# Kernel optimization log

Measured on AMD Instinct MI355X. Metric: run time of the kernel, lower is better.

The kernel has to match this reference:

```python
import jax, jax.numpy as jnp
import numpy as np

B, N, D = 256, 128, 128            # batch, tree nodes (incl. zero-pad node 0), input_feature_dim
MAX_PRED, MAX_COL, MAX_OP = 30, 200, 20
OTHER = D - 2 * MAX_PRED - 1 - 32  # 35
C_IN = D + 64 - 2 * MAX_PRED - 1   # 131 = tree-conv input channels


def setup_inputs() -> dict:
    key = jax.random.key(0)
    ks = jax.random.split(key, 14)
    others = jax.random.normal(ks[0], (B, N, OTHER), dtype=jnp.float32)
    cols = jax.random.randint(ks[1], (B, N, MAX_PRED), 0, MAX_COL).astype(jnp.float32)
    ops = jax.random.randint(ks[2], (B, N, MAX_PRED), 0, MAX_OP).astype(jnp.float32)
    length = jax.random.randint(ks[3], (B, N, 1), 0, MAX_PRED + 1).astype(jnp.float32)
    param = jax.random.normal(ks[4], (B, N, 32), dtype=jnp.float32)
    feature = jnp.concatenate([others, cols, ops, length, param], axis=-1).transpose(0, 2, 1)  # (B, D, N)
    indexes = jax.random.randint(ks[5], (B, 3 * (N - 1), 1), 0, N, dtype=jnp.int32).astype(jnp.int64)

    def conv_w(k, o, i):
        return jax.random.normal(k, (o, i, 3), dtype=jnp.float32) * (1.0 / np.sqrt(3 * i))

    def lin_w(k, o, i):
        return jax.random.normal(k, (o, i), dtype=jnp.float32) * (1.0 / np.sqrt(i))

    return dict(
        feature=feature, indexes=indexes,
        col_embed=jax.random.normal(ks[6], (MAX_COL, 32), dtype=jnp.float32),
        op_embed=jax.random.normal(ks[7], (MAX_OP, 32), dtype=jnp.float32),
        w1=conv_w(ks[8], 256, C_IN), b1=jnp.zeros((256,), jnp.float32),
        w2=conv_w(ks[9], 128, 256), b2=jnp.zeros((128,), jnp.float32),
        w3=conv_w(ks[10], 64, 128), b3=jnp.zeros((64,), jnp.float32),
        fw1=lin_w(ks[11], 32, 64), fb1=jnp.zeros((32,), jnp.float32),
        fw2=lin_w(ks[12], 1, 32), fb2=jnp.zeros((1,), jnp.float32),
    )


def tree_conv(x, idx, w, b):
    # x: (B, C, N); idx: (B, 3M, 1) with M = N-1; w: (O, C, 3)
    Bb, C, _ = x.shape
    g = jnp.take_along_axis(x, idx[:, :, 0][:, None, :], axis=2)        # (B, C, 3M) gather (self,left,right)
    g = g.reshape(Bb, C, -1, 3)                                          # (B, C, M, 3)
    out = jnp.einsum('bcmk,ock->bom', g, w) + b[None, :, None]           # stride-3 kernel-3 conv
    zero = jnp.zeros((Bb, w.shape[0], 1), out.dtype)                     # re-prepend zero-pad node
    return jnp.concatenate([zero, out], axis=2)                          # (B, O, N)


def tree_norm(x):
    # per-sample layernorm over (channel, node) dims, unbiased std (torch.std default)
    mean = jnp.mean(x, axis=(1, 2), keepdims=True)
    std = jnp.std(x, axis=(1, 2), ddof=1, keepdims=True)
    return (x - mean) / (std + 1e-5)


def reference(feature, indexes, col_embed, op_embed, w1, b1, w2, b2, w3, b3, fw1, fb1, fw2, fb2):
    Bb, d, n = feature.shape
    f = feature.transpose(0, 2, 1).reshape(Bb * n, d)
    others = f[:, :OTHER]
    cols = jax.lax.stop_gradient(f[:, OTHER:OTHER + MAX_PRED]).astype(jnp.int32)
    ops = jax.lax.stop_gradient(f[:, OTHER + MAX_PRED:OTHER + 2 * MAX_PRED]).astype(jnp.int32)
    length = f[:, OTHER + 2 * MAX_PRED:OTHER + 2 * MAX_PRED + 1]          # (BN, 1)
    param = f[:, -32:]
    emb = jnp.concatenate([col_embed[cols], op_embed[ops]], axis=-1)      # (BN, P, 64)
    mask = jnp.arange(MAX_PRED)[None, :] < length                         # (BN, P)
    total = jnp.sum(emb * mask[..., None], axis=1)                        # (BN, 64) masked sum
    collate = jnp.concatenate([others, total, param], axis=-1).reshape(Bb, n, -1).transpose(0, 2, 1)  # (B, C_IN, N)

    x = jax.nn.leaky_relu(tree_norm(tree_conv(collate, indexes, w1, b1)), 0.01)
    x = jax.nn.leaky_relu(tree_norm(tree_conv(x, indexes, w2, b2)), 0.01)
    x = tree_norm(tree_conv(x, indexes, w3, b3))                          # (B, 64, N)
    pooled = jnp.max(x, axis=2)                                           # DynamicPooling -> (B, 64)
    h = jax.nn.relu(pooled @ fw1.T + fb1)
    return h @ fw2.T + fb2                                                # (B, 1)
```

## Files before the change

### kernel.cpp

```cpp
#include <hip/hip_runtime.h>
#include <hip/hip_bf16.h>
#include <math.h>

#define B_    256
#define N_    128
#define MAXP  30
#define OTHER_ 35
#define CIN1  131
#define NIDX  381

#define KPAD1 160
#define KPAD2 256
#define KPAD3 128
#define S_IDX (B_ * NIDX)
#define S_P1  (15 * 4 * 4 * 512)
#define S_P2  (24 * 4 * 2 * 512)
#define S_P3  (12 * 4 * 1 * 512)
#define PREP_TOTAL (S_IDX + S_P1 + S_P2 + S_P3)
#define PREP_BLOCKS ((PREP_TOTAL + 511) / 512)

typedef short short8 __attribute__((ext_vector_type(8)));
typedef float f32x4 __attribute__((ext_vector_type(4)));

__device__ inline void split1(float v, short& h, short& l) {
  unsigned u = __float_as_uint(v);
  unsigned hb = (u + 0x7fffu + ((u >> 16) & 1u)) >> 16;
  float fh = __uint_as_float(hb << 16);
  float r = v - fh;
  unsigned u2 = __float_as_uint(r);
  unsigned lb = (u2 + 0x7fffu + ((u2 >> 16) & 1u)) >> 16;
  h = (short)hb;
  l = (short)lb;
}

__device__ inline void split2(float v, short& h, short& l) {
  __hip_bfloat16 hb = __float2bfloat16(v);
  float fh = __bfloat162float(hb);
  __hip_bfloat16 lb = __float2bfloat16(v - fh);
  __builtin_memcpy(&h, &hb, 2);
  __builtin_memcpy(&l, &lb, 2);
}

template <int KREAL, int KPAD, int SUB, int NWO>
__device__ inline void packw(int l, const float* __restrict__ w,
                             short* __restrict__ oh, short* __restrict__ ol) {
  const int e = l & 7;
  const int lane = (l >> 3) & 63;
  const int x = l >> 9;
  const int su = x % SUB;
  const int y = x / SUB;
  const int g = y % NWO;
  const int gks = y / NWO;
  const int oc = (g * SUB + su) * 16 + (lane & 15);
  const int ctot = gks * 32 + ((lane >> 4) & 3) * 8 + e;
  const int kk = ctot / KPAD;
  const int ch = ctot - kk * KPAD;
  const float v = (ch < KREAL) ? w[(oc * KREAL + ch) * 3 + kk] : 0.f;
  short h, lo;
  split1(v, h, lo);
  oh[l] = h;
  ol[l] = lo;
}

__global__ __launch_bounds__(512) void prep_kernel(
    const void* __restrict__ rawIdx, int* __restrict__ idx32,
    const float* __restrict__ w1, short* __restrict__ w1h, short* __restrict__ w1l,
    const float* __restrict__ w2, short* __restrict__ w2h, short* __restrict__ w2l,
    const float* __restrict__ w3, short* __restrict__ w3h, short* __restrict__ w3l) {
  const int gid = blockIdx.x * 512 + threadIdx.x;
  if (gid < S_IDX) {
    const int* r32 = (const int*)rawIdx;
    const int lane = threadIdx.x & 63;
    const int lo = r32[2 * lane];
    const int hi = r32[2 * lane + 1];
    const bool ok = (hi == 0 && lo >= 0 && lo < N_);
    const bool is64 = __all(ok);
    idx32[gid] = is64 ? (int)((const long long*)rawIdx)[gid] : ((const int*)rawIdx)[gid];
  } else if (gid < S_IDX + S_P1) {
    packw<131, KPAD1, 4, 4>(gid - S_IDX, w1, w1h, w1l);
  } else if (gid < S_IDX + S_P1 + S_P2) {
    packw<256, KPAD2, 2, 4>(gid - (S_IDX + S_P1), w2, w2h, w2l);
  } else if (gid < PREP_TOTAL) {
    packw<128, KPAD3, 1, 4>(gid - (S_IDX + S_P1 + S_P2), w3, w3h, w3l);
  }
}

__global__ __launch_bounds__(1024, 1) void fused_kernel(
    const float* __restrict__ feature,
    const float* __restrict__ col_embed,
    const float* __restrict__ op_embed,
    const int* __restrict__ idx,
    const short* __restrict__ w1h, const short* __restrict__ w1l,
    const short* __restrict__ w2h, const short* __restrict__ w2l,
    const short* __restrict__ w3h, const short* __restrict__ w3l,
    const float* __restrict__ b1, const float* __restrict__ b2,
    const float* __restrict__ b3,
    const float* __restrict__ fw1, const float* __restrict__ fb1,
    const float* __restrict__ fw2, const float* __restrict__ fb2,
    float* __restrict__ out) {
  constexpr int CINP = 264;

  __shared__ short smem[128 * CINP * 2];
  __shared__ int nb_s[NIDX];
  __shared__ double red[32];
  __shared__ float bc[2];
  __shared__ float poolw[16][16];

  short* sH = smem;
  short* sL = smem + 128 * CINP;
  float* feat = (float*)smem;
  float* ceL  = ((float*)smem) + 128 * 133;
  float* oeL  = ceL + 200 * 32;

  const int b = blockIdx.x;
  const int tid = threadIdx.x;
  const int lane = tid & 63;
  const int w = tid >> 6;
  const int wj = w >> 2;
  const int wo = w & 3;
  const int col = lane & 15;
  const int grp = (lane >> 4) & 3;
  const int jbase = wj * 32;
  const int cl = lane & 31;

  const short8* __restrict__ wp1h = (const short8*)w1h;
  const short8* __restrict__ wp1l = (const short8*)w1l;
  const short8* __restrict__ wp2h = (const short8*)w2h;
  const short8* __restrict__ wp2l = (const short8*)w2l;
  const short8* __restrict__ wp3h = (const short8*)w3h;
  const short8* __restrict__ wp3l = (const short8*)w3l;

  auto blockStats = [&](double ss, double sq, double cnt) {
#pragma unroll
    for (int o = 32; o > 0; o >>= 1) {
      ss += __shfl_down(ss, o, 64);
      sq += __shfl_down(sq, o, 64);
    }
    if (lane == 0) { red[w * 2] = ss; red[w * 2 + 1] = sq; }
    __syncthreads();
    if (tid == 0) {
      double S = 0.0, Q = 0.0;
#pragma unroll
      for (int i = 0; i < 16; ++i) { S += red[i * 2]; Q += red[i * 2 + 1]; }
      const double m = S / cnt;
      double var = (Q - S * S / cnt) / (cnt - 1.0);
      if (var < 0.0) var = 0.0;
      bc[0] = (float)m;
      bc[1] = (float)(1.0 / (sqrt(var) + 1e-5));
    }
    __syncthreads();
  };

  {
    const float* fb = feature + (size_t)b * 16384;
#pragma unroll
    for (int it = 0; it < 4; ++it) {
      const int t = it * 1024 + tid;
      const int d = t >> 5;
      const int c4 = (t & 31) * 4;
      const float4 v = *reinterpret_cast<const float4*>(&fb[d * 128 + c4]);
      float* p = &feat[d * 133 + c4];
      p[0] = v.x; p[1] = v.y; p[2] = v.z; p[3] = v.w;
    }
    const float4* s = (const float4*)col_embed;
    float4* d4 = (float4*)ceL;
#pragma unroll
    for (int it = 0; it < 2; ++it) {
      const int t = it * 1024 + tid;
      if (t < 1600) d4[t] = s[t];
    }
    if (tid < 160) ((float4*)oeL)[tid] = ((const float4*)op_embed)[tid];
    if (tid < NIDX) nb_s[tid] = idx[b * NIDX + tid];
  }
  __syncthreads();

  float emb[8], oth[8], par[8];
#pragma unroll
  for (int ni = 0; ni < 8; ++ni) {
    const int n = w * 8 + ni;
    int civ = 0, oiv = 0;
    if (lane < MAXP) civ = (int)feat[(OTHER_ + lane) * 133 + n];
    if (lane >= 32 && lane < 32 + MAXP) oiv = (int)feat[(OTHER_ + MAXP + (lane - 32)) * 133 + n];
    const int L = (int)feat[95 * 133 + n];
    float acc = 0.f;
    for (int i = 0; i < L; ++i) {
      const int cv = __shfl(civ, i);
      const int ov = __shfl(oiv, 32 + i);
      acc += (lane < 32) ? ceL[cv * 32 + cl] : oeL[ov * 32 + cl];
    }
    emb[ni] = acc;
    oth[ni] = (lane < 35) ? feat[lane * 133 + n] : 0.f;
    par[ni] = (lane < 32) ? feat[(96 + lane) * 133 + n] : 0.f;
  }
  int nbr[2][3];
#pragma unroll
  for (int jt = 0; jt < 2; ++jt) {
    const int jA = jbase + jt * 16 + col;
#pragma unroll
    for (int kk = 0; kk < 3; ++kk)
      nbr[jt][kk] = (jA > 0) ? nb_s[(jA - 1) * 3 + kk] : 0;
  }
  __syncthreads();

#pragma unroll
  for (int ni = 0; ni < 8; ++ni) {
    const int n = w * 8 + ni;
    const int base = n * CINP;
    short h, l;
    split2(emb[ni], h, l);
    sH[base + 35 + lane] = h; sL[base + 35 + lane] = l;
    if (lane < 35) {
      split2(oth[ni], h, l);
      sH[base + lane] = h; sL[base + lane] = l;
    }
    if (lane < 32) {
      split2(par[ni], h, l);
      sH[base + 99 + lane] = h; sL[base + 99 + lane] = l;
    }
    if (lane < 29) { sH[base + 131 + lane] = 0; sL[base + 131 + lane] = 0; }
  }
  __syncthreads();

  f32x4 a1[2][4];
#pragma unroll
  for (int jt = 0; jt < 2; ++jt)
#pragma unroll
    for (int su = 0; su < 4; ++su) {
      a1[jt][su][0] = 0.f; a1[jt][su][1] = 0.f;
      a1[jt][su][2] = 0.f; a1[jt][su][3] = 0.f;
    }

#pragma unroll
  for (int kk = 0; kk < 3; ++kk) {
#pragma unroll
    for (int ks = 0; ks < 5; ++ks) {
      const int gks = kk * 5 + ks;
      short8 ah[2], al[2];
#pragma unroll
      for (int jt = 0; jt < 2; ++jt) {
        const int ei = nbr[jt][kk] * CINP + ks * 32 + grp * 8;
        ah[jt] = *reinterpret_cast<const short8*>(&sH[ei]);
        al[jt] = *reinterpret_cast<const short8*>(&sL[ei]);
      }
      short8 bh[4], bl[4];
#pragma unroll
      for (int su = 0; su < 4; ++su) {
        const int wi = ((gks * 4 + wo) * 4 + su) * 64 + lane;
        bh[su] = wp1h[wi];
        bl[su] = wp1l[wi];
      }
#pragma unroll
      for (int jt = 0; jt < 2; ++jt)
#pragma unroll
        for (int su = 0; su < 4; ++su) {
          a1[jt][su] = __builtin_amdgcn_mfma_f32_16x16x32_bf16(ah[jt], bh[su], a1[jt][su], 0, 0, 0);
          a1[jt][su] = __builtin_amdgcn_mfma_f32_16x16x32_bf16(al[jt], bh[su], a1[jt][su], 0, 0, 0);
          a1[jt][su] = __builtin_amdgcn_mfma_f32_16x16x32_bf16(ah[jt], bl[su], a1[jt][su], 0, 0, 0);
        }
    }
  }

  {
    double ss = 0.0, sq = 0.0;
#pragma unroll
    for (int su = 0; su < 4; ++su) {
      const float bv = b1[(wo * 4 + su) * 16 + col];
#pragma unroll
      for (int jt = 0; jt < 2; ++jt)
#pragma unroll
        for (int r = 0; r < 4; ++r) {
          const int j = jbase + jt * 16 + grp * 4 + r;
          const float val = (j > 0) ? a1[jt][su][r] + bv : 0.f;
          a1[jt][su][r] = val;
          ss += (double)val;
          sq += (double)val * (double)val;
        }
    }
    blockStats(ss, sq, 256.0 * 128.0);
  }
  const float mean1 = bc[0], inv1 = bc[1];

#pragma unroll
  for (int su = 0; su < 4; ++su) {
    const int c = (wo * 4 + su) * 16 + col;
#pragma unroll
    for (int jt = 0; jt < 2; ++jt)
#pragma unroll
      for (int r = 0; r < 4; ++r) {
        const int j = jbase + jt * 16 + grp * 4 + r;
        float v = (a1[jt][su][r] - mean1) * inv1;
        v = fmaxf(v, 0.01f * v);
        short h, l;
        split2(v, h, l);
        sH[j * CINP + c] = h;
        sL[j * CINP + c] = l;
      }
  }
  __syncthreads();

  f32x4 a2[2][2];
#pragma unroll
  for (int jt = 0; jt < 2; ++jt)
#pragma unroll
    for (int su = 0; su < 2; ++su) {
      a2[jt][su][0] = 0.f; a2[jt][su][1] = 0.f;
      a2[jt][su][2] = 0.f; a2[jt][su][3] = 0.f;
    }

#pragma unroll
  for (int kk = 0; kk < 3; ++kk) {
#pragma unroll
    for (int ks = 0; ks < 8; ++ks) {
      const int gks = kk * 8 + ks;
      short8 ah[2], al[2];
#pragma unroll
      for (int jt = 0; jt < 2; ++jt) {
        const int ei = nbr[jt][kk] * CINP + ks * 32 + grp * 8;
        ah[jt] = *reinterpret_cast<const short8*>(&sH[ei]);
        al[jt] = *reinterpret_cast<const short8*>(&sL[ei]);
      }
      short8 bh[2], bl[2];
#pragma unroll
      for (int su = 0; su < 2; ++su) {
        const int wi = ((gks * 4 + wo) * 2 + su) * 64 + lane;
        bh[su] = wp2h[wi];
        bl[su] = wp2l[wi];
      }
#pragma unroll
      for (int jt = 0; jt < 2; ++jt)
#pragma unroll
        for (int su = 0; su < 2; ++su) {
          a2[jt][su] = __builtin_amdgcn_mfma_f32_16x16x32_bf16(ah[jt], bh[su], a2[jt][su], 0, 0, 0);
          a2[jt][su] = __builtin_amdgcn_mfma_f32_16x16x32_bf16(al[jt], bh[su], a2[jt][su], 0, 0, 0);
          a2[jt][su] = __builtin_amdgcn_mfma_f32_16x16x32_bf16(ah[jt], bl[su], a2[jt][su], 0, 0, 0);
        }
    }
  }

  {
    double ss = 0.0, sq = 0.0;
#pragma unroll
    for (int su = 0; su < 2; ++su) {
      const float bv = b2[(wo * 2 + su) * 16 + col];
#pragma unroll
      for (int jt = 0; jt < 2; ++jt)
#pragma unroll
        for (int r = 0; r < 4; ++r) {
          const int j = jbase + jt * 16 + grp * 4 + r;
          const float val = (j > 0) ? a2[jt][su][r] + bv : 0.f;
          a2[jt][su][r] = val;
          ss += (double)val;
          sq += (double)val * (double)val;
        }
    }
    blockStats(ss, sq, 128.0 * 128.0);
  }
  const float mean2 = bc[0], inv2 = bc[1];

#pragma unroll
  for (int su = 0; su < 2; ++su) {
    const int c = (wo * 2 + su) * 16 + col;
#pragma unroll
    for (int jt = 0; jt < 2; ++jt)
#pragma unroll
      for (int r = 0; r < 4; ++r) {
        const int j = jbase + jt * 16 + grp * 4 + r;
        float v = (a2[jt][su][r] - mean2) * inv2;
        v = fmaxf(v, 0.01f * v);
        short h, l;
        split2(v, h, l);
        sH[j * CINP + c] = h;
        sL[j * CINP + c] = l;
      }
  }
  __syncthreads();

  f32x4 a3[2];
#pragma unroll
  for (int jt = 0; jt < 2; ++jt) {
    a3[jt][0] = 0.f; a3[jt][1] = 0.f; a3[jt][2] = 0.f; a3[jt][3] = 0.f;
  }

#pragma unroll
  for (int kk = 0; kk < 3; ++kk) {
#pragma unroll
    for (int ks = 0; ks < 4; ++ks) {
      const int gks = kk * 4 + ks;
      short8 ah[2], al[2];
#pragma unroll
      for (int jt = 0; jt < 2; ++jt) {
        const int ei = nbr[jt][kk] * CINP + ks * 32 + grp * 8;
        ah[jt] = *reinterpret_cast<const short8*>(&sH[ei]);
        al[jt] = *reinterpret_cast<const short8*>(&sL[ei]);
      }
      short8 bh, bl;
      {
        const int wi = (gks * 4 + wo) * 64 + lane;
        bh = wp3h[wi];
        bl = wp3l[wi];
      }
#pragma unroll
      for (int jt = 0; jt < 2; ++jt) {
        a3[jt] = __builtin_amdgcn_mfma_f32_16x16x32_bf16(ah[jt], bh, a3[jt], 0, 0, 0);
        a3[jt] = __builtin_amdgcn_mfma_f32_16x16x32_bf16(al[jt], bh, a3[jt], 0, 0, 0);
        a3[jt] = __builtin_amdgcn_mfma_f32_16x16x32_bf16(ah[jt], bl, a3[jt], 0, 0, 0);
      }
    }
  }

  {
    double ss = 0.0, sq = 0.0;
    const float bv = b3[wo * 16 + col];
#pragma unroll
    for (int jt = 0; jt < 2; ++jt)
#pragma unroll
      for (int r = 0; r < 4; ++r) {
        const int j = jbase + jt * 16 + grp * 4 + r;
        const float val = (j > 0) ? a3[jt][r] + bv : 0.f;
        a3[jt][r] = val;
        ss += (double)val;
        sq += (double)val * (double)val;
      }
    blockStats(ss, sq, 64.0 * 128.0);
  }
  const float mean3 = bc[0], inv3 = bc[1];

  {
    float pm = -3.4e38f;
#pragma unroll
    for (int jt = 0; jt < 2; ++jt)
#pragma unroll
      for (int r = 0; r < 4; ++r)
        pm = fmaxf(pm, (a3[jt][r] - mean3) * inv3);
    pm = fmaxf(pm, __shfl_xor(pm, 16, 64));
    pm = fmaxf(pm, __shfl_xor(pm, 32, 64));
    if (lane < 16) poolw[w][col] = pm;
  }
  __syncthreads();

  if (w == 0) {
    float hval = 0.f;
    if (lane < 32) {
      float a = fb1[lane];
#pragma unroll 8
      for (int c = 0; c < 64; ++c) {
        const int oq = c >> 4, oc16 = c & 15;
        float p = poolw[oq][oc16];
#pragma unroll
        for (int jw = 1; jw < 4; ++jw) p = fmaxf(p, poolw[jw * 4 + oq][oc16]);
        a = fmaf(p, fw1[lane * 64 + c], a);
      }
      hval = fmaxf(a, 0.f) * fw2[lane];
    }
#pragma unroll
    for (int o = 32; o > 0; o >>= 1) hval += __shfl_down(hval, o, 64);
    if (lane == 0) out[b] = hval + fb2[0];
  }
}

extern "C" void kernel_launch(void* const* d_in, const int* in_sizes, int n_in,
                              void* d_out, int out_size, void* d_ws, size_t ws_size,
                              hipStream_t stream) {
  const float* feature   = (const float*)d_in[0];
  const void*  indexes   = d_in[1];
  const float* col_embed = (const float*)d_in[2];
  const float* op_embed  = (const float*)d_in[3];
  const float* w1  = (const float*)d_in[4];
  const float* b1  = (const float*)d_in[5];
  const float* w2  = (const float*)d_in[6];
  const float* b2  = (const float*)d_in[7];
  const float* w3  = (const float*)d_in[8];
  const float* b3  = (const float*)d_in[9];
  const float* fw1 = (const float*)d_in[10];
  const float* fb1 = (const float*)d_in[11];
  const float* fw2 = (const float*)d_in[12];
  const float* fb2 = (const float*)d_in[13];
  float* out = (float*)d_out;

  char* ws = (char*)d_ws;
  size_t off = 0;
  auto carve = [&](size_t bytes) -> char* {
    off = (off + 255) & ~(size_t)255;
    char* p = ws + off;
    off += bytes;
    return p;
  };
  int*   idx32 = (int*)carve((size_t)S_IDX * sizeof(int));
  short* w1h   = (short*)carve((size_t)S_P1 * sizeof(short));
  short* w1l   = (short*)carve((size_t)S_P1 * sizeof(short));
  short* w2h   = (short*)carve((size_t)S_P2 * sizeof(short));
  short* w2l   = (short*)carve((size_t)S_P2 * sizeof(short));
  short* w3h   = (short*)carve((size_t)S_P3 * sizeof(short));
  short* w3l   = (short*)carve((size_t)S_P3 * sizeof(short));
  (void)ws_size; (void)in_sizes; (void)n_in; (void)out_size;

  hipLaunchKernelGGL(prep_kernel, dim3(PREP_BLOCKS), dim3(512), 0, stream,
                     indexes, idx32, w1, w1h, w1l, w2, w2h, w2l, w3, w3h, w3l);
  hipLaunchKernelGGL(fused_kernel, dim3(B_), dim3(1024), 0, stream,
                     feature, col_embed, op_embed, idx32,
                     w1h, w1l, w2h, w2l, w3h, w3l,
                     b1, b2, b3, fw1, fb1, fw2, fb2, out);
}
```

Before: 79.41 us.

## Retile warps to 8 node-groups by 2 output-channel groups

The warp-to-tile mapping changes from 4 node blocks × 4 output-channel blocks (32 nodes each) to 8 node blocks × 2 output-channel blocks (16 nodes each). The weight packing layout is changed to match. Each warp now loads one gathered A fragment per k-step and reuses it across more output tiles, which cuts shared-memory gather reads. The trade-off is that each warp fetches twice as many weight fragments from global or L2 memory. The pooling reduction and final MLP indexing are rewritten for the new layout.

```diff
diff --git a/kernel.cpp b/kernel.cpp
--- a/kernel.cpp
+++ b/kernel.cpp
@@ -13,9 +13,9 @@
 #define KPAD2 256
 #define KPAD3 128
 #define S_IDX (B_ * NIDX)
-#define S_P1  (15 * 4 * 4 * 512)
-#define S_P2  (24 * 4 * 2 * 512)
-#define S_P3  (12 * 4 * 1 * 512)
+#define S_P1  (15 * 2 * 8 * 512)
+#define S_P2  (24 * 2 * 4 * 512)
+#define S_P3  (12 * 2 * 2 * 512)
 #define PREP_TOTAL (S_IDX + S_P1 + S_P2 + S_P3)
 #define PREP_BLOCKS ((PREP_TOTAL + 511) / 512)
 
@@ -77,11 +77,11 @@
     const bool is64 = __all(ok);
     idx32[gid] = is64 ? (int)((const long long*)rawIdx)[gid] : ((const int*)rawIdx)[gid];
   } else if (gid < S_IDX + S_P1) {
-    packw<131, KPAD1, 4, 4>(gid - S_IDX, w1, w1h, w1l);
+    packw<131, KPAD1, 8, 2>(gid - S_IDX, w1, w1h, w1l);
   } else if (gid < S_IDX + S_P1 + S_P2) {
-    packw<256, KPAD2, 2, 4>(gid - (S_IDX + S_P1), w2, w2h, w2l);
+    packw<256, KPAD2, 4, 2>(gid - (S_IDX + S_P1), w2, w2h, w2l);
   } else if (gid < PREP_TOTAL) {
-    packw<128, KPAD3, 1, 4>(gid - (S_IDX + S_P1 + S_P2), w3, w3h, w3l);
+    packw<128, KPAD3, 2, 2>(gid - (S_IDX + S_P1 + S_P2), w3, w3h, w3l);
   }
 }
 
@@ -104,7 +104,7 @@
   __shared__ int nb_s[NIDX];
   __shared__ double red[32];
   __shared__ float bc[2];
-  __shared__ float poolw[16][16];
+  __shared__ float poolw[16][32];
 
   short* sH = smem;
   short* sL = smem + 128 * CINP;
@@ -116,11 +116,11 @@
   const int tid = threadIdx.x;
   const int lane = tid & 63;
   const int w = tid >> 6;
-  const int wj = w >> 2;
-  const int wo = w & 3;
+  const int wj = w >> 1;
+  const int wo = w & 1;
   const int col = lane & 15;
   const int grp = (lane >> 4) & 3;
-  const int jbase = wj * 32;
+  const int jbase = wj * 16;
   const int cl = lane & 31;
 
   const short8* __restrict__ wp1h = (const short8*)w1h;
@@ -192,13 +192,12 @@
     oth[ni] = (lane < 35) ? feat[lane * 133 + n] : 0.f;
     par[ni] = (lane < 32) ? feat[(96 + lane) * 133 + n] : 0.f;
   }
-  int nbr[2][3];
-#pragma unroll
-  for (int jt = 0; jt < 2; ++jt) {
-    const int jA = jbase + jt * 16 + col;
+  int nbr[3];
+  {
+    const int jA = jbase + col;
 #pragma unroll
     for (int kk = 0; kk < 3; ++kk)
-      nbr[jt][kk] = (jA > 0) ? nb_s[(jA - 1) * 3 + kk] : 0;
+      nbr[kk] = (jA > 0) ? nb_s[(jA - 1) * 3 + kk] : 0;
   }
   __syncthreads();
 
@@ -221,119 +220,166 @@
   }
   __syncthreads();
 
-  f32x4 a1[2][4];
-#pragma unroll
-  for (int jt = 0; jt < 2; ++jt)
-#pragma unroll
-    for (int su = 0; su < 4; ++su) {
-      a1[jt][su][0] = 0.f; a1[jt][su][1] = 0.f;
-      a1[jt][su][2] = 0.f; a1[jt][su][3] = 0.f;
-    }
+  f32x4 a1[8];
+#pragma unroll
+  for (int su = 0; su < 8; ++su) {
+    a1[su][0] = 0.f; a1[su][1] = 0.f; a1[su][2] = 0.f; a1[su][3] = 0.f;
+  }
 
 #pragma unroll
   for (int kk = 0; kk < 3; ++kk) {
 #pragma unroll
     for (int ks = 0; ks < 5; ++ks) {
       const int gks = kk * 5 + ks;
-      short8 ah[2], al[2];
-#pragma unroll
-      for (int jt = 0; jt < 2; ++jt) {
-        const int ei = nbr[jt][kk] * CINP + ks * 32 + grp * 8;
-        ah[jt] = *reinterpret_cast<const short8*>(&sH[ei]);
-        al[jt] = *reinterpret_cast<const short8*>(&sL[ei]);
-      }
-      short8 bh[4], bl[4];
-#pragma unroll
-      for (int su = 0; su < 4; ++su) {
-        const int wi = ((gks * 4 + wo) * 4 + su) * 64 + lane;
-        bh[su] = wp1h[wi];
-        bl[su] = wp1l[wi];
-      }
-#pragma unroll
-      for (int jt = 0; jt < 2; ++jt)
-#pragma unroll
-        for (int su = 0; su < 4; ++su) {
-          a1[jt][su] = __builtin_amdgcn_mfma_f32_16x16x32_bf16(ah[jt], bh[su], a1[jt][su], 0, 0, 0);
-          a1[jt][su] = __builtin_amdgcn_mfma_f32_16x16x32_bf16(al[jt], bh[su], a1[jt][su], 0, 0, 0);
-          a1[jt][su] = __builtin_amdgcn_mfma_f32_16x16x32_bf16(ah[jt], bl[su], a1[jt][su], 0, 0, 0);
+      const int ei = nbr[kk] * CINP + ks * 32 + grp * 8;
+      const short8 ah = *reinterpret_cast<const short8*>(&sH[ei]);
+      const short8 al = *reinterpret_cast<const short8*>(&sL[ei]);
+#pragma unroll
+      for (int sc = 0; sc < 2; ++sc) {
+        short8 bh[4], bl[4];
+#pragma unroll
+        for (int u = 0; u < 4; ++u) {
+          const int su = sc * 4 + u;
+          const int wi = ((gks * 2 + wo) * 8 + su) * 64 + lane;
+          bh[u] = wp1h[wi];
+          bl[u] = wp1l[wi];
         }
+#pragma unroll
+        for (int u = 0; u < 4; ++u) {
+          const int su = sc * 4 + u;
+          a1[su] = __builtin_amdgcn_mfma_f32_16x16x32_bf16(ah, bh[u], a1[su], 0, 0, 0);
+          a1[su] = __builtin_amdgcn_mfma_f32_16x16x32_bf16(al, bh[u], a1[su], 0, 0, 0);
+          a1[su] = __builtin_amdgcn_mfma_f32_16x16x32_bf16(ah, bl[u], a1[su], 0, 0, 0);
+        }
+      }
     }
   }
 
   {
     double ss = 0.0, sq = 0.0;
 #pragma unroll
+    for (int su = 0; su < 8; ++su) {
+      const float bv = b1[(wo * 8 + su) * 16 + col];
+#pragma unroll
+      for (int r = 0; r < 4; ++r) {
+        const int j = jbase + grp * 4 + r;
+        const float val = (j > 0) ? a1[su][r] + bv : 0.f;
+        a1[su][r] = val;
+        ss += (double)val;
+        sq += (double)val * (double)val;
+      }
+    }
+    blockStats(ss, sq, 256.0 * 128.0);
+  }
+  const float mean1 = bc[0], inv1 = bc[1];
+
+#pragma unroll
+  for (int su = 0; su < 8; ++su) {
+    const int c = (wo * 8 + su) * 16 + col;
+#pragma unroll
+    for (int r = 0; r < 4; ++r) {
+      const int j = jbase + grp * 4 + r;
+      float v = (a1[su][r] - mean1) * inv1;
+      v = fmaxf(v, 0.01f * v);
+      short h, l;
+      split2(v, h, l);
+      sH[j * CINP + c] = h;
+      sL[j * CINP + c] = l;
+    }
+  }
+  __syncthreads();
+
+  f32x4 a2[4];
+#pragma unroll
+  for (int su = 0; su < 4; ++su) {
+    a2[su][0] = 0.f; a2[su][1] = 0.f; a2[su][2] = 0.f; a2[su][3] = 0.f;
+  }
+
+#pragma unroll
+  for (int kk = 0; kk < 3; ++kk) {
+#pragma unroll
+    for (int ks = 0; ks < 8; ++ks) {
+      const int gks = kk * 8 + ks;
+      const int ei = nbr[kk] * CINP + ks * 32 + grp * 8;
+      const short8 ah = *reinterpret_cast<const short8*>(&sH[ei]);
+      const short8 al = *reinterpret_cast<const short8*>(&sL[ei]);
+      short8 bh[4], bl[4];
+#pragma unroll
+      for (int su = 0; su < 4; ++su) {
+        const int wi = ((gks * 2 + wo) * 4 + su) * 64 + lane;
+        bh[su] = wp2h[wi];
+        bl[su] = wp2l[wi];
+      }
+#pragma unroll
+      for (int su = 0; su < 4; ++su) {
+        a2[su] = __builtin_amdgcn_mfma_f32_16x16x32_bf16(ah, bh[su], a2[su], 0, 0, 0);
+        a2[su] = __builtin_amdgcn_mfma_f32_16x16x32_bf16(al, bh[su], a2[su], 0, 0, 0);
+        a2[su] = __builtin_amdgcn_mfma_f32_16x16x32_bf16(ah, bl[su], a2[su], 0, 0, 0);
+      }
+    }
+  }
+
+  {
+    double ss = 0.0, sq = 0.0;
+#pragma unroll
     for (int su = 0; su < 4; ++su) {
-      const float bv = b1[(wo * 4 + su) * 16 + col];
-#pragma unroll
-      for (int jt = 0; jt < 2; ++jt)
-#pragma unroll
-        for (int r = 0; r < 4; ++r) {
-          const int j = jbase + jt * 16 + grp * 4 + r;
-          const float val = (j > 0) ? a1[jt][su][r] + bv : 0.f;
-          a1[jt][su][r] = val;
-          ss += (double)val;
-          sq += (double)val * (double)val;
-        }
-    }
-    blockStats(ss, sq, 256.0 * 128.0);
-  }
-  const float mean1 = bc[0], inv1 = bc[1];
+      const float bv = b2[(wo * 4 + su) * 16 + col];
+#pragma unroll
+      for (int r = 0; r < 4; ++r) {
+        const int j = jbase + grp * 4 + r;
+        const float val = (j > 0) ? a2[su][r] + bv : 0.f;
+        a2[su][r] = val;
+        ss += (double)val;
+        sq += (double)val * (double)val;
+      }
+    }
+    blockStats(ss, sq, 128.0 * 128.0);
+  }
+  const float mean2 = bc[0], inv2 = bc[1];
 
 #pragma unroll
   for (int su = 0; su < 4; ++su) {
     const int c = (wo * 4 + su) * 16 + col;
 #pragma unroll
-    for (int jt = 0; jt < 2; ++jt)
-#pragma unroll
-      for (int r = 0; r < 4; ++r) {
-        const int j = jbase + jt * 16 + grp * 4 + r;
-        float v = (a1[jt][su][r] - mean1) * inv1;
-        v = fmaxf(v, 0.01f * v);
-        short h, l;
-        split2(v, h, l);
-        sH[j * CINP + c] = h;
-        sL[j * CINP + c] = l;
-      }
-  }
-  __syncthreads();
-
-  f32x4 a2[2][2];
-#pragma unroll
-  for (int jt = 0; jt < 2; ++jt)
-#pragma unroll
-    for (int su = 0; su < 2; ++su) {
-      a2[jt][su][0] = 0.f; a2[jt][su][1] = 0.f;
-      a2[jt][su][2] = 0.f; a2[jt][su][3] = 0.f;
-    }
+    for (int r = 0; r < 4; ++r) {
+      const int j = jbase + grp * 4 + r;
+      float v = (a2[su][r] - mean2) * inv2;
+      v = fmaxf(v, 0.01f * v);
+      short h, l;
+      split2(v, h, l);
+      sH[j * CINP + c] = h;
+      sL[j * CINP + c] = l;
+    }
+  }
+  __syncthreads();
+
+  f32x4 a3[2];
+#pragma unroll
+  for (int su = 0; su < 2; ++su) {
+    a3[su][0] = 0.f; a3[su][1] = 0.f; a3[su][2] = 0.f; a3[su][3] = 0.f;
+  }
 
 #pragma unroll
   for (int kk = 0; kk < 3; ++kk) {
 #pragma unroll
-    for (int ks = 0; ks < 8; ++ks) {
-      const int gks = kk * 8 + ks;
-      short8 ah[2], al[2];
-#pragma unroll
-      for (int jt = 0; jt < 2; ++jt) {
-        const int ei = nbr[jt][kk] * CINP + ks * 32 + grp * 8;
-        ah[jt] = *reinterpret_cast<const short8*>(&sH[ei]);
-        al[jt] = *reinterpret_cast<const short8*>(&sL[ei]);
-      }
+    for (int ks = 0; ks < 4; ++ks) {
+      const int gks = kk * 4 + ks;
+      const int ei = nbr[kk] * CINP + ks * 32 + grp * 8;
+      const short8 ah = *reinterpret_cast<const short8*>(&sH[ei]);
+      const short8 al = *reinterpret_cast<const short8*>(&sL[ei]);
       short8 bh[2], bl[2];
 #pragma unroll
       for (int su = 0; su < 2; ++su) {
-        const int wi = ((gks * 4 + wo) * 2 + su) * 64 + lane;
-        bh[su] = wp2h[wi];
-        bl[su] = wp2l[wi];
-      }
-#pragma unroll
-      for (int jt = 0; jt < 2; ++jt)
-#pragma unroll
-        for (int su = 0; su < 2; ++su) {
-          a2[jt][su] = __builtin_amdgcn_mfma_f32_16x16x32_bf16(ah[jt], bh[su], a2[jt][su], 0, 0, 0);
-          a2[jt][su] = __builtin_amdgcn_mfma_f32_16x16x32_bf16(al[jt], bh[su], a2[jt][su], 0, 0, 0);
-          a2[jt][su] = __builtin_amdgcn_mfma_f32_16x16x32_bf16(ah[jt], bl[su], a2[jt][su], 0, 0, 0);
-        }
+        const int wi = ((gks * 2 + wo) * 2 + su) * 64 + lane;
+        bh[su] = wp3h[wi];
+        bl[su] = wp3l[wi];
+      }
+#pragma unroll
+      for (int su = 0; su < 2; ++su) {
+        a3[su] = __builtin_amdgcn_mfma_f32_16x16x32_bf16(ah, bh[su], a3[su], 0, 0, 0);
+        a3[su] = __builtin_amdgcn_mfma_f32_16x16x32_bf16(al, bh[su], a3[su], 0, 0, 0);
+        a3[su] = __builtin_amdgcn_mfma_f32_16x16x32_bf16(ah, bl[su], a3[su], 0, 0, 0);
+      }
     }
   }
 
@@ -341,100 +387,29 @@
     double ss = 0.0, sq = 0.0;
 #pragma unroll
     for (int su = 0; su < 2; ++su) {
-      const float bv = b2[(wo * 2 + su) * 16 + col];
-#pragma unroll
-      for (int jt = 0; jt < 2; ++jt)
-#pragma unroll
-        for (int r = 0; r < 4; ++r) {
-          const int j = jbase + jt * 16 + grp * 4 + r;
-          const float val = (j > 0) ? a2[jt][su][r] + bv : 0.f;
-          a2[jt][su][r] = val;
-          ss += (double)val;
-          sq += (double)val * (double)val;
-        }
-    }
-    blockStats(ss, sq, 128.0 * 128.0);
-  }
-  const float mean2 = bc[0], inv2 = bc[1];
-
-#pragma unroll
-  for (int su = 0; su < 2; ++su) {
-    const int c = (wo * 2 + su) * 16 + col;
-#pragma unroll
-    for (int jt = 0; jt < 2; ++jt)
+      const float bv = b3[(wo * 2 + su) * 16 + col];
 #pragma unroll
       for (int r = 0; r < 4; ++r) {
-        const int j = jbase + jt * 16 + grp * 4 + r;
-        float v = (a2[jt][su][r] - mean2) * inv2;
-        v = fmaxf(v, 0.01f * v);
-        short h, l;
-        split2(v, h, l);
-        sH[j * CINP + c] = h;
-        sL[j * CINP + c] = l;
-      }
-  }
-  __syncthreads();
-
-  f32x4 a3[2];
-#pragma unroll
-  for (int jt = 0; jt < 2; ++jt) {
-    a3[jt][0] = 0.f; a3[jt][1] = 0.f; a3[jt][2] = 0.f; a3[jt][3] = 0.f;
-  }
-
-#pragma unroll
-  for (int kk = 0; kk < 3; ++kk) {
-#pragma unroll
-    for (int ks = 0; ks < 4; ++ks) {
-      const int gks = kk * 4 + ks;
-      short8 ah[2], al[2];
-#pragma unroll
-      for (int jt = 0; jt < 2; ++jt) {
-        const int ei = nbr[jt][kk] * CINP + ks * 32 + grp * 8;
-        ah[jt] = *reinterpret_cast<const short8*>(&sH[ei]);
-        al[jt] = *reinterpret_cast<const short8*>(&sL[ei]);
-      }
-      short8 bh, bl;
-      {
-        const int wi = (gks * 4 + wo) * 64 + lane;
-        bh = wp3h[wi];
-        bl = wp3l[wi];
-      }
-#pragma unroll
-      for (int jt = 0; jt < 2; ++jt) {
-        a3[jt] = __builtin_amdgcn_mfma_f32_16x16x32_bf16(ah[jt], bh, a3[jt], 0, 0, 0);
-        a3[jt] = __builtin_amdgcn_mfma_f32_16x16x32_bf16(al[jt], bh, a3[jt], 0, 0, 0);
-        a3[jt] = __builtin_amdgcn_mfma_f32_16x16x32_bf16(ah[jt], bl, a3[jt], 0, 0, 0);
-      }
-    }
-  }
-
-  {
-    double ss = 0.0, sq = 0.0;
-    const float bv = b3[wo * 16 + col];
-#pragma unroll
-    for (int jt = 0; jt < 2; ++jt)
-#pragma unroll
-      for (int r = 0; r < 4; ++r) {
-        const int j = jbase + jt * 16 + grp * 4 + r;
-        const float val = (j > 0) ? a3[jt][r] + bv : 0.f;
-        a3[jt][r] = val;
+        const int j = jbase + grp * 4 + r;
+        const float val = (j > 0) ? a3[su][r] + bv : 0.f;
+        a3[su][r] = val;
         ss += (double)val;
         sq += (double)val * (double)val;
       }
+    }
     blockStats(ss, sq, 64.0 * 128.0);
   }
   const float mean3 = bc[0], inv3 = bc[1];
 
-  {
+#pragma unroll
+  for (int su = 0; su < 2; ++su) {
     float pm = -3.4e38f;
 #pragma unroll
-    for (int jt = 0; jt < 2; ++jt)
-#pragma unroll
-      for (int r = 0; r < 4; ++r)
-        pm = fmaxf(pm, (a3[jt][r] - mean3) * inv3);
+    for (int r = 0; r < 4; ++r)
+      pm = fmaxf(pm, (a3[su][r] - mean3) * inv3);
     pm = fmaxf(pm, __shfl_xor(pm, 16, 64));
     pm = fmaxf(pm, __shfl_xor(pm, 32, 64));
-    if (lane < 16) poolw[w][col] = pm;
+    if (lane < 16) poolw[w][su * 16 + col] = pm;
   }
   __syncthreads();
 
@@ -444,10 +419,10 @@
       float a = fb1[lane];
 #pragma unroll 8
       for (int c = 0; c < 64; ++c) {
-        const int oq = c >> 4, oc16 = c & 15;
-        float p = poolw[oq][oc16];
-#pragma unroll
-        for (int jw = 1; jw < 4; ++jw) p = fmaxf(p, poolw[jw * 4 + oq][oc16]);
+        const int half = c >> 5, loc = c & 31;
+        float p = poolw[half][loc];
+#pragma unroll
+        for (int jw = 1; jw < 8; ++jw) p = fmaxf(p, poolw[jw * 2 + half][loc]);
         a = fmaf(p, fw1[lane * 64 + c], a);
       }
       hval = fmaxf(a, 0.f) * fw2[lane];
```

Measured after the change: 104.2 us. +31.2%, slower.
